# Optimization experiments

Hardware: AMD Instinct MI355X
Metric: run time of the kernel (lower is better)

## Reference

```python
import jax, jax.numpy as jnp
import numpy as np

EPS = 1e-08

def _masked_stats(x, m, denom):
    # x: [B,C,H,W] already multiplied by mask; m: [B,1,H,W]; denom: [B,1,1,1]
    mean = jnp.sum(x, axis=(2, 3), keepdims=True) / denom          # [B,C,1,1]
    var = jnp.sum(((x - mean) * m) ** 2, axis=(2, 3), keepdims=True) / denom
    return mean, jnp.maximum(var, 0.0)

def _modulate(w, a, b):
    # concat [B,C,1,1]+[B,C,1,1] -> [B,2C], linear (no bias), back to [B,C,1,1]
    v = jnp.concatenate([a, b], axis=1)[:, :, 0, 0]                # [B,2C]
    y = v @ w.T                                                    # [B,C]
    return y[:, :, None, None]

def setup_inputs() -> dict:
    key = jax.random.key(0)
    ks = jax.random.split(key, 7)
    B, C, H, W = 4, 128, 256, 256
    x1 = jax.random.normal(ks[0], (B, C, H, W), dtype=jnp.float32)
    x2 = jax.random.normal(ks[1], (B, C, H, W), dtype=jnp.float32)
    mask = jax.random.uniform(ks[2], (B, 1, H // 2, W // 2), dtype=jnp.float32)
    w_in_mean = jax.random.normal(ks[3], (C, 2 * C), dtype=jnp.float32) * 0.05
    w_in_var = jax.random.normal(ks[4], (C, 2 * C), dtype=jnp.float32) * 0.05
    w_out_mean = jax.random.normal(ks[5], (C, 2 * C), dtype=jnp.float32) * 0.05
    w_out_var = jax.random.normal(ks[6], (C, 2 * C), dtype=jnp.float32) * 0.05
    return {"x1": x1, "x2": x2, "mask": mask,
            "w_in_mean": w_in_mean, "w_in_var": w_in_var,
            "w_out_mean": w_out_mean, "w_out_var": w_out_var}

def reference(x1, x2, mask, w_in_mean, w_in_var, w_out_mean, w_out_var):
    H, W = x1.shape[2], x1.shape[3]
    # nearest-neighbor upsample of mask to x1 spatial size (integer factor)
    rh, rw = H // mask.shape[2], W // mask.shape[3]
    m = jnp.repeat(jnp.repeat(mask, rh, axis=2), rw, axis=3)       # [B,1,H,W]
    om = 1.0 - m
    n_in = jnp.sum(m, axis=(2, 3), keepdims=True) + EPS            # [B,1,1,1]
    n_out = jnp.sum(om, axis=(2, 3), keepdims=True) + EPS

    x1_in, x2_in = x1 * m, x2 * m
    x1_out, x2_out = x1 * om, x2 * om

    x1_in_mean, x1_in_var = _masked_stats(x1_in, m, n_in)
    x2_in_mean, x2_in_var = _masked_stats(x2_in, m, n_in)
    x1_out_mean, x1_out_var = _masked_stats(x1_out, om, n_out)
    x2_out_mean, x2_out_var = _masked_stats(x2_out, om, n_out)

    ada_in_mean = _modulate(w_in_mean, x1_in_mean, x2_in_mean)
    ada_in_var = _modulate(w_in_var, x1_in_var, x2_in_var)
    ada_out_mean = _modulate(w_out_mean, x1_out_mean, x2_out_mean)
    ada_out_var = _modulate(w_out_var, x1_out_var, x2_out_var)

    norm_in = (x1_in - x1_in_mean) * jax.lax.rsqrt(x1_in_var + EPS)
    norm_out = (x1_out - x1_out_mean) * jax.lax.rsqrt(x1_out_var + EPS)
    ada_x1_in = norm_in * ada_in_var + ada_in_mean
    ada_x1_out = norm_out * ada_out_var + ada_out_mean
    return ada_x1_in * m + ada_x1_out * om
```

## Files before the change

### kernel.cpp

```cpp
#include <hip/hip_runtime.h>

#define EPS 1e-8f

using f32x4 = __attribute__((ext_vector_type(4))) float;

__global__ __launch_bounds__(256) void k_stats(
    const float* __restrict__ x1,
    const float* __restrict__ x2,
    const float* __restrict__ mask,
    float* __restrict__ stats)
{
    int blk = blockIdx.x;
    int s   = blk & 1;
    int bc  = blk >> 1;
    int b   = bc >> 7;
    int tid = threadIdx.x;

    const size_t poff = (size_t)bc * 65536 + (size_t)s * 32768;
    const float* xp1 = x1 + poff;
    const float* xp2 = x2 + poff;
    const float* mp  = mask + b * 16384;
    const int gi0 = s * 32768 + tid * 8;

    float a[12];
#pragma unroll
    for (int j = 0; j < 12; ++j) a[j] = 0.f;

    int off0 = tid * 8;
    f32x4 c1a = *(const f32x4*)(xp1 + off0);
    f32x4 c1b = *(const f32x4*)(xp1 + off0 + 4);
    f32x4 c2a = *(const f32x4*)(xp2 + off0);
    f32x4 c2b = *(const f32x4*)(xp2 + off0 + 4);
    int h0 = gi0 >> 8, w0 = gi0 & 255;
    f32x4 cm = *(const f32x4*)(mp + (h0 >> 1) * 128 + (w0 >> 1));

    for (int g = 0; g < 16; ++g) {
        f32x4 n1a, n1b, n2a, n2b, nm;
        if (g < 15) {
            int off = (g + 1) * 2048 + tid * 8;
            int gi  = gi0 + (g + 1) * 2048;
            int h = gi >> 8, w = gi & 255;
            n1a = *(const f32x4*)(xp1 + off);
            n1b = *(const f32x4*)(xp1 + off + 4);
            n2a = *(const f32x4*)(xp2 + off);
            n2b = *(const f32x4*)(xp2 + off + 4);
            nm  = *(const f32x4*)(mp + (h >> 1) * 128 + (w >> 1));
        }
#pragma unroll
        for (int j = 0; j < 8; ++j) {
            float m  = cm[j >> 1];
            float om = 1.f - m;
            float m2 = m * m, om2 = om * om;
            float f1 = (j < 4) ? c1a[j & 3] : c1b[j & 3];
            float f2 = (j < 4) ? c2a[j & 3] : c2b[j & 3];
            float p1 = f1 * m2,  p2 = f2 * m2;
            a[0] += f1 * m;  a[1] += p1 * m;  a[2] += p1 * p1;
            a[3] += f2 * m;  a[4] += p2 * m;  a[5] += p2 * p2;
            float q1 = f1 * om2, q2 = f2 * om2;
            a[6] += f1 * om; a[7] += q1 * om; a[8] += q1 * q1;
            a[9] += f2 * om; a[10]+= q2 * om; a[11]+= q2 * q2;
        }
        c1a = n1a; c1b = n1b; c2a = n2a; c2b = n2b; cm = nm;
    }

#pragma unroll
    for (int j = 0; j < 12; ++j)
#pragma unroll
        for (int d = 32; d > 0; d >>= 1)
            a[j] += __shfl_down(a[j], d, 64);

    __shared__ float red[4][12];
    int wv = tid >> 6, ln = tid & 63;
    if (ln == 0) {
#pragma unroll
        for (int j = 0; j < 12; ++j) red[wv][j] = a[j];
    }
    __syncthreads();
    if (tid < 12) {
        float v = red[0][tid] + red[1][tid] + red[2][tid] + red[3][tid];
        stats[(size_t)blk * 12 + tid] = v;
    }
}

__global__ __launch_bounds__(256) void k_mod(
    const float* __restrict__ mask,
    const float* __restrict__ w_in_mean,
    const float* __restrict__ w_in_var,
    const float* __restrict__ w_out_mean,
    const float* __restrict__ w_out_var,
    const float* __restrict__ stats,
    float* __restrict__ derived)
{
    int b   = blockIdx.x;
    int tid = threadIdx.x;

    const float* mp = mask + b * 16384;
    float sm = 0.f, sm2 = 0.f;
    for (int it = 0; it < 16; ++it) {
        const f32x4 mv = *(const f32x4*)(mp + (it * 256 + tid) * 4);
#pragma unroll
        for (int j = 0; j < 4; ++j) { float m = mv[j]; sm += m; sm2 += m * m; }
    }
#pragma unroll
    for (int d = 32; d > 0; d >>= 1) {
        sm  += __shfl_down(sm, d, 64);
        sm2 += __shfl_down(sm2, d, 64);
    }
    __shared__ float rr[8];
    __shared__ float SMs, SM2s;
    int wv = tid >> 6, ln = tid & 63;
    if (ln == 0) { rr[wv] = sm; rr[4 + wv] = sm2; }
    __syncthreads();
    if (tid == 0) {
        SMs  = 4.f * (rr[0] + rr[1] + rr[2] + rr[3]);
        SM2s = 4.f * (rr[4] + rr[5] + rr[6] + rr[7]);
    }
    __syncthreads();
    float SM = SMs, SM2 = SM2s;
    float n_in  = SM + EPS;
    float n_out = 65536.f - SM + EPS;
    float SOM2  = 65536.f - 2.f * SM + SM2;

    __shared__ float vin_mean[256], vin_var[256], vout_mean[256], vout_var[256];

    if (tid < 128) {
        int c = tid;
        const float* st = stats + (size_t)(b * 128 + c) * 2 * 12;
        float s[12];
#pragma unroll
        for (int j = 0; j < 12; ++j) s[j] = st[j] + st[12 + j];
        float mi1 = s[0] / n_in;
        float vi1 = fmaxf((s[2] - 2.f * mi1 * s[1] + mi1 * mi1 * SM2) / n_in, 0.f);
        float mi2 = s[3] / n_in;
        float vi2 = fmaxf((s[5] - 2.f * mi2 * s[4] + mi2 * mi2 * SM2) / n_in, 0.f);
        float mo1 = s[6] / n_out;
        float vo1 = fmaxf((s[8] - 2.f * mo1 * s[7] + mo1 * mo1 * SOM2) / n_out, 0.f);
        float mo2 = s[9] / n_out;
        float vo2 = fmaxf((s[11] - 2.f * mo2 * s[10] + mo2 * mo2 * SOM2) / n_out, 0.f);
        vin_mean[c] = mi1;  vin_mean[128 + c] = mi2;
        vin_var[c]  = vi1;  vin_var[128 + c]  = vi2;
        vout_mean[c] = mo1; vout_mean[128 + c] = mo2;
        vout_var[c]  = vo1; vout_var[128 + c]  = vo2;
        float* d = derived + (size_t)(b * 128 + c) * 8;
        d[0] = mi1; d[1] = rsqrtf(vi1 + EPS);
        d[2] = mo1; d[3] = rsqrtf(vo1 + EPS);
    }
    __syncthreads();

    for (int t = tid; t < 512; t += 256) {
        int mat = t >> 7, row = t & 127;
        const float* wp;
        const float* vec;
        if (mat == 0)      { wp = w_in_mean;  vec = vin_mean; }
        else if (mat == 1) { wp = w_in_var;   vec = vin_var; }
        else if (mat == 2) { wp = w_out_mean; vec = vout_mean; }
        else               { wp = w_out_var;  vec = vout_var; }
        wp += row * 256;
        float acc = 0.f;
        for (int k = 0; k < 256; k += 4) {
            f32x4 wv4 = *(const f32x4*)(wp + k);
#pragma unroll
            for (int j = 0; j < 4; ++j) acc += wv4[j] * vec[k + j];
        }
        derived[(size_t)(b * 128 + row) * 8 + 4 + mat] = acc;
    }
}

__global__ __launch_bounds__(256) void k_apply(
    const float* __restrict__ x1,
    const float* __restrict__ mask,
    const float* __restrict__ derived,
    float* __restrict__ out)
{
    int blk   = blockIdx.x;
    int bc    = blk >> 2;
    int chunk = blk & 3;
    int b     = bc >> 7;
    const float* d = derived + (size_t)bc * 8;
    float mean_in = d[0], inv_in = d[1], mean_out = d[2], inv_out = d[3];
    float am_in = d[4], av_in = d[5], am_out = d[6], av_out = d[7];
    float ci1 = inv_in * av_in;
    float ci0 = am_in - mean_in * ci1;
    float co1 = inv_out * av_out;
    float co0 = am_out - mean_out * co1;

    int tid = threadIdx.x;
    const float* xp = x1 + (size_t)bc * 65536;
    float* op = out + (size_t)bc * 65536;
    const float* mp = mask + b * 16384;
    const int gi0 = chunk * 16384 + tid * 8;

    f32x4 cxa = *(const f32x4*)(xp + gi0);
    f32x4 cxb = *(const f32x4*)(xp + gi0 + 4);
    int h0 = gi0 >> 8, w0 = gi0 & 255;
    f32x4 cm = *(const f32x4*)(mp + (h0 >> 1) * 128 + (w0 >> 1));

    for (int g = 0; g < 8; ++g) {
        f32x4 nxa, nxb, nm;
        if (g < 7) {
            int gi = gi0 + (g + 1) * 2048;
            int h = gi >> 8, w = gi & 255;
            nxa = *(const f32x4*)(xp + gi);
            nxb = *(const f32x4*)(xp + gi + 4);
            nm  = *(const f32x4*)(mp + (h >> 1) * 128 + (w >> 1));
        }
        f32x4 oa, ob;
#pragma unroll
        for (int j = 0; j < 8; ++j) {
            float m  = cm[j >> 1];
            float om = 1.f - m;
            float x  = (j < 4) ? cxa[j & 3] : cxb[j & 3];
            float r  = x * (m * m * ci1 + om * om * co1) + ci0 * m + co0 * om;
            if (j < 4) oa[j & 3] = r; else ob[j & 3] = r;
        }
        int go = gi0 + g * 2048;
        __builtin_nontemporal_store(oa, (f32x4*)(op + go));
        __builtin_nontemporal_store(ob, (f32x4*)(op + go + 4));
        cxa = nxa; cxb = nxb; cm = nm;
    }
}

extern "C" void kernel_launch(void* const* d_in, const int* in_sizes, int n_in,
                              void* d_out, int out_size, void* d_ws, size_t ws_size,
                              hipStream_t stream) {
    const float* x1        = (const float*)d_in[0];
    const float* x2        = (const float*)d_in[1];
    const float* mask      = (const float*)d_in[2];
    const float* w_in_mean = (const float*)d_in[3];
    const float* w_in_var  = (const float*)d_in[4];
    const float* w_out_mean= (const float*)d_in[5];
    const float* w_out_var = (const float*)d_in[6];

    float* stats   = (float*)d_ws;
    float* derived = stats + 1024 * 12;
    float* out = (float*)d_out;

    k_stats<<<512 * 2, 256, 0, stream>>>(x1, x2, mask, stats);
    k_mod<<<4, 256, 0, stream>>>(mask, w_in_mean, w_in_var, w_out_mean, w_out_var,
                                 stats, derived);
    k_apply<<<512 * 4, 256, 0, stream>>>(x1, mask, derived, out);
}
```

Baseline: 373.5 us.

## Split stats into quarter-plane blocks and parallelize modulation across matrices

k_stats now uses four blocks per (b,c) plane instead of two, each covering 16384 elements, so there are twice as many smaller blocks; k_mod sums four partial stats. k_mod now launches 16 blocks, one per batch and weight matrix, and each GEMV row is split across two lanes joined with a shuffle. Launch bounds hint occupancy 8 on the stats and apply kernels. The aim is better load balance and more latency hiding in the stats pass and a shorter serial modulation step, at the cost of recomputing the mask sums in each of the 16 k_mod blocks.

```diff
diff --git a/kernel.cpp b/kernel.cpp
--- a/kernel.cpp
+++ b/kernel.cpp
@@ -4,23 +4,23 @@
 
 using f32x4 = __attribute__((ext_vector_type(4))) float;
 
-__global__ __launch_bounds__(256) void k_stats(
+__global__ __launch_bounds__(256, 8) void k_stats(
     const float* __restrict__ x1,
     const float* __restrict__ x2,
     const float* __restrict__ mask,
     float* __restrict__ stats)
 {
-    int blk = blockIdx.x;
-    int s   = blk & 1;
-    int bc  = blk >> 1;
-    int b   = bc >> 7;
-    int tid = threadIdx.x;
-
-    const size_t poff = (size_t)bc * 65536 + (size_t)s * 32768;
+    int blk   = blockIdx.x;
+    int chunk = blk & 3;
+    int bc    = blk >> 2;
+    int b     = bc >> 7;
+    int tid   = threadIdx.x;
+
+    const size_t poff = (size_t)bc * 65536 + (size_t)chunk * 16384;
     const float* xp1 = x1 + poff;
     const float* xp2 = x2 + poff;
     const float* mp  = mask + b * 16384;
-    const int gi0 = s * 32768 + tid * 8;
+    const int gi0 = chunk * 16384 + tid * 8;
 
     float a[12];
 #pragma unroll
@@ -34,9 +34,9 @@
     int h0 = gi0 >> 8, w0 = gi0 & 255;
     f32x4 cm = *(const f32x4*)(mp + (h0 >> 1) * 128 + (w0 >> 1));
 
-    for (int g = 0; g < 16; ++g) {
+    for (int g = 0; g < 8; ++g) {
         f32x4 n1a, n1b, n2a, n2b, nm;
-        if (g < 15) {
+        if (g < 7) {
             int off = (g + 1) * 2048 + tid * 8;
             int gi  = gi0 + (g + 1) * 2048;
             int h = gi >> 8, w = gi & 255;
@@ -91,7 +91,8 @@
     const float* __restrict__ stats,
     float* __restrict__ derived)
 {
-    int b   = blockIdx.x;
+    int b   = blockIdx.x >> 2;
+    int mat = blockIdx.x & 3;
     int tid = threadIdx.x;
 
     const float* mp = mask + b * 16384;
@@ -121,14 +122,15 @@
     float n_out = 65536.f - SM + EPS;
     float SOM2  = 65536.f - 2.f * SM + SM2;
 
-    __shared__ float vin_mean[256], vin_var[256], vout_mean[256], vout_var[256];
+    __shared__ float vec[256];
 
     if (tid < 128) {
         int c = tid;
-        const float* st = stats + (size_t)(b * 128 + c) * 2 * 12;
+        const float* st = stats + (size_t)(b * 128 + c) * 4 * 12;
         float s[12];
 #pragma unroll
-        for (int j = 0; j < 12; ++j) s[j] = st[j] + st[12 + j];
+        for (int j = 0; j < 12; ++j)
+            s[j] = (st[j] + st[12 + j]) + (st[24 + j] + st[36 + j]);
         float mi1 = s[0] / n_in;
         float vi1 = fmaxf((s[2] - 2.f * mi1 * s[1] + mi1 * mi1 * SM2) / n_in, 0.f);
         float mi2 = s[3] / n_in;
@@ -137,36 +139,38 @@
         float vo1 = fmaxf((s[8] - 2.f * mo1 * s[7] + mo1 * mo1 * SOM2) / n_out, 0.f);
         float mo2 = s[9] / n_out;
         float vo2 = fmaxf((s[11] - 2.f * mo2 * s[10] + mo2 * mo2 * SOM2) / n_out, 0.f);
-        vin_mean[c] = mi1;  vin_mean[128 + c] = mi2;
-        vin_var[c]  = vi1;  vin_var[128 + c]  = vi2;
-        vout_mean[c] = mo1; vout_mean[128 + c] = mo2;
-        vout_var[c]  = vo1; vout_var[128 + c]  = vo2;
-        float* d = derived + (size_t)(b * 128 + c) * 8;
-        d[0] = mi1; d[1] = rsqrtf(vi1 + EPS);
-        d[2] = mo1; d[3] = rsqrtf(vo1 + EPS);
-    }
-    __syncthreads();
-
-    for (int t = tid; t < 512; t += 256) {
-        int mat = t >> 7, row = t & 127;
-        const float* wp;
-        const float* vec;
-        if (mat == 0)      { wp = w_in_mean;  vec = vin_mean; }
-        else if (mat == 1) { wp = w_in_var;   vec = vin_var; }
-        else if (mat == 2) { wp = w_out_mean; vec = vout_mean; }
-        else               { wp = w_out_var;  vec = vout_var; }
-        wp += row * 256;
-        float acc = 0.f;
-        for (int k = 0; k < 256; k += 4) {
-            f32x4 wv4 = *(const f32x4*)(wp + k);
-#pragma unroll
-            for (int j = 0; j < 4; ++j) acc += wv4[j] * vec[k + j];
-        }
+        float v0, v1;
+        if (mat == 0)      { v0 = mi1; v1 = mi2; }
+        else if (mat == 1) { v0 = vi1; v1 = vi2; }
+        else if (mat == 2) { v0 = mo1; v1 = mo2; }
+        else               { v0 = vo1; v1 = vo2; }
+        vec[c] = v0; vec[128 + c] = v1;
+        if (mat == 0) {
+            float* d = derived + (size_t)(b * 128 + c) * 8;
+            d[0] = mi1; d[1] = rsqrtf(vi1 + EPS);
+            d[2] = mo1; d[3] = rsqrtf(vo1 + EPS);
+        }
+    }
+    __syncthreads();
+
+    const float* wp = (mat == 0) ? w_in_mean :
+                      (mat == 1) ? w_in_var :
+                      (mat == 2) ? w_out_mean : w_out_var;
+    int row = tid >> 1, half = tid & 1;
+    const float* wr = wp + row * 256 + half * 128;
+    const float* vp = vec + half * 128;
+    float acc = 0.f;
+    for (int k = 0; k < 128; k += 4) {
+        f32x4 w4 = *(const f32x4*)(wr + k);
+#pragma unroll
+        for (int j = 0; j < 4; ++j) acc += w4[j] * vp[k + j];
+    }
+    acc += __shfl_xor(acc, 1, 64);
+    if (half == 0)
         derived[(size_t)(b * 128 + row) * 8 + 4 + mat] = acc;
-    }
-}
-
-__global__ __launch_bounds__(256) void k_apply(
+}
+
+__global__ __launch_bounds__(256, 8) void k_apply(
     const float* __restrict__ x1,
     const float* __restrict__ mask,
     const float* __restrict__ derived,
@@ -232,11 +236,11 @@
     const float* w_out_var = (const float*)d_in[6];
 
     float* stats   = (float*)d_ws;
-    float* derived = stats + 1024 * 12;
+    float* derived = stats + 2048 * 12;
     float* out = (float*)d_out;
 
-    k_stats<<<512 * 2, 256, 0, stream>>>(x1, x2, mask, stats);
-    k_mod<<<4, 256, 0, stream>>>(mask, w_in_mean, w_in_var, w_out_mean, w_out_var,
-                                 stats, derived);
+    k_stats<<<512 * 4, 256, 0, stream>>>(x1, x2, mask, stats);
+    k_mod<<<4 * 4, 256, 0, stream>>>(mask, w_in_mean, w_in_var, w_out_mean, w_out_var,
+                                     stats, derived);
     k_apply<<<512 * 4, 256, 0, stream>>>(x1, mask, derived, out);
 }
```

Result: slower. 410.2 us (+9.8%).
